# Kernel optimization log

Measured on AMD Instinct MI355X. Metric: run time of the kernel, lower is better.

Reference implementation:

```python
import jax, jax.numpy as jnp
import numpy as np

HIDDEN = 4096
N_HEADS = 32
HEAD_DIM = HIDDEN // N_HEADS  # 128
ROPE_BASE = 10000.0


def _rotate_half(x):
    h = x.shape[-1] // 2
    return jnp.concatenate((-x[..., h:], x[..., :h]), axis=-1)


def _rope_sin_cos(position_ids):
    # position_ids: [B, S] int -> sin, cos: [B, 1, S, head_dim]
    inv_freq = 1.0 / (ROPE_BASE ** (jnp.arange(0, HEAD_DIM, 2, dtype=jnp.float32) / HEAD_DIM))
    freqs = position_ids.astype(jnp.float32)[..., None] * inv_freq  # [B,S,hd/2]
    emb = jnp.concatenate((freqs, freqs), axis=-1)  # [B,S,hd]
    return jnp.sin(emb)[:, None, :, :], jnp.cos(emb)[:, None, :, :]


def setup_inputs() -> dict:
    key = jax.random.key(0)
    k1, k2, k3 = jax.random.split(key, 3)
    B, S = 2, 2048
    hidden_states = jax.random.normal(k1, (B, S, HIDDEN), dtype=jnp.float32)
    w_qkv = jax.random.normal(k2, (HIDDEN, 3 * HIDDEN), dtype=jnp.float32) * 0.02
    wo = jax.random.normal(k3, (HIDDEN, HIDDEN), dtype=jnp.float32) * 0.02
    position_ids = jnp.broadcast_to(jnp.arange(S, dtype=jnp.int32)[None, :], (B, S))
    return {"hidden_states": hidden_states, "w_qkv": w_qkv, "wo": wo,
            "position_ids": position_ids}


def reference(hidden_states, w_qkv, wo, position_ids):
    B, S, H = hidden_states.shape
    qkv = hidden_states @ w_qkv  # [B,S,3H]
    q, k, v = jnp.split(qkv, 3, axis=-1)
    # [B,S,nH,hd] -> [B,nH,S,hd]
    q = q.reshape(B, S, N_HEADS, HEAD_DIM).transpose(0, 2, 1, 3)
    k = k.reshape(B, S, N_HEADS, HEAD_DIM).transpose(0, 2, 1, 3)
    v = v.reshape(B, S, N_HEADS, HEAD_DIM).transpose(0, 2, 1, 3)
    sin, cos = _rope_sin_cos(position_ids)  # [B,1,S,hd]
    q = q * cos + _rotate_half(q) * sin
    k = k * cos + _rotate_half(k) * sin
    scale = 1.0 / np.sqrt(HEAD_DIM)
    scores = jnp.einsum('bhqd,bhkd->bhqk', q, k) * scale
    causal = jnp.tril(jnp.ones((S, S), dtype=bool))
    scores = jnp.where(causal[None, None, :, :], scores, jnp.finfo(scores.dtype).min)
    attn = jax.nn.softmax(scores, axis=-1)
    out = jnp.einsum('bhqk,bhkd->bhqd', attn, v)  # [B,nH,S,hd]
    out = out.transpose(0, 2, 1, 3).reshape(B, S, H)
    return out @ wo
```

## Files before the change

kernel.cpp:

```cpp
#include <hip/hip_runtime.h>

typedef unsigned int u32;
typedef unsigned short u16;
typedef short short8 __attribute__((ext_vector_type(8)));
typedef float f32x4 __attribute__((ext_vector_type(4)));
typedef unsigned short us4 __attribute__((ext_vector_type(4)));

#define S_LEN 2048
#define BATCH 2
#define HID 4096
#define NH 32
#define HD 128
#define TRIH 12288

#define GCAST(p) ((const __attribute__((address_space(1))) u32*)(p))
#define LCAST(p) ((__attribute__((address_space(3))) u32*)(p))

static __device__ __forceinline__ u16 f2bf(float f) {
  union { float f; u32 u; } x; x.f = f;
  u32 u = x.u;
  u32 r = u + 0x7FFFu + ((u >> 16) & 1u);
  return (u16)(r >> 16);
}
static __device__ __forceinline__ float bf2f(u16 h) {
  union { u32 u; float f; } x; x.u = ((u32)h) << 16;
  return x.f;
}

__global__ __launch_bounds__(256) void cvt_f32_bf16(const float* __restrict__ in,
                                                    u16* __restrict__ out, int n4) {
  int i = blockIdx.x * 256 + threadIdx.x;
  if (i >= n4) return;
  float4 v = ((const float4*)in)[i];
  us4 o;
  o.x = f2bf(v.x); o.y = f2bf(v.y); o.z = f2bf(v.z); o.w = f2bf(v.w);
  ((us4*)out)[i] = o;
}

__global__ __launch_bounds__(256) void tr_cvt(const float* __restrict__ in,
                                              u16* __restrict__ out, int R, int C) {
  __shared__ float tile[32][33];
  int c0 = blockIdx.x * 32, r0 = blockIdx.y * 32;
  int tx = threadIdx.x, ty = threadIdx.y;
  for (int i = ty; i < 32; i += 8)
    tile[i][tx] = in[(size_t)(r0 + i) * C + c0 + tx];
  __syncthreads();
  for (int i = ty; i < 32; i += 8)
    out[(size_t)(c0 + i) * R + r0 + tx] = f2bf(tile[tx][i]);
}


template<int MQ, int NQ>
static __device__ __forceinline__ void mfma_quad(f32x4 (&acc)[8][4], short8 (&af)[4][2],
                                                 short8 (&bfr)[4][2]) {
#pragma unroll
  for (int ml = 0; ml < 4; ++ml)
#pragma unroll
    for (int nl = 0; nl < 2; ++nl) {
      acc[MQ*4+ml][NQ*2+nl] = __builtin_amdgcn_mfma_f32_16x16x32_bf16(
          af[ml][0], bfr[NQ*2+nl][0], acc[MQ*4+ml][NQ*2+nl], 0, 0, 0);
      acc[MQ*4+ml][NQ*2+nl] = __builtin_amdgcn_mfma_f32_16x16x32_bf16(
          af[ml][1], bfr[NQ*2+nl][1], acc[MQ*4+ml][NQ*2+nl], 0, 0, 0);
    }
}

template<int MQ>
static __device__ __forceinline__ void read_a(short8 (&af)[4][2], const u16* abase, int lane) {
#pragma unroll
  for (int ml = 0; ml < 4; ++ml) {
    int r = MQ*64 + ml*16 + (lane & 15);
#pragma unroll
    for (int kh = 0; kh < 2; ++kh) {
      int j = kh*4 + (lane >> 4);
      af[ml][kh] = *(const short8*)(abase + r*64 + ((j ^ (r & 7)) << 3));
    }
  }
}
template<int NQ>
static __device__ __forceinline__ void read_b(short8 (&bfr)[4][2], const u16* bbase,
                                              int rbase, int lane) {
#pragma unroll
  for (int nl = 0; nl < 2; ++nl) {
    int r = rbase + (NQ*2+nl)*16 + (lane & 15);
#pragma unroll
    for (int kh = 0; kh < 2; ++kh) {
      int j = kh*4 + (lane >> 4);
      bfr[NQ*2+nl][kh] = *(const short8*)(bbase + r*64 + ((j ^ (r & 7)) << 3));
    }
  }
}

#define BAR_MFMA(MQX, NQX) \
  __builtin_amdgcn_s_barrier(); \
  asm volatile("s_waitcnt lgkmcnt(0)" ::: "memory"); \
  __builtin_amdgcn_sched_barrier(0); \
  __builtin_amdgcn_s_setprio(1); \
  mfma_quad<MQX, NQX>(acc, af, bfr); \
  __builtin_amdgcn_s_setprio(0); \
  __builtin_amdgcn_s_barrier();

#define BAR_MFMA_DRAIN(MQX, NQX, NSTR) \
  __builtin_amdgcn_s_barrier(); \
  asm volatile("s_waitcnt lgkmcnt(0)" ::: "memory"); \
  __builtin_amdgcn_sched_barrier(0); \
  __builtin_amdgcn_s_setprio(1); \
  mfma_quad<MQX, NQX>(acc, af, bfr); \
  __builtin_amdgcn_s_setprio(0); \
  asm volatile("s_waitcnt vmcnt(" NSTR ")" ::: "memory"); \
  __builtin_amdgcn_s_barrier(); \
  __builtin_amdgcn_sched_barrier(0);

template<int OUTF32>
__global__ __launch_bounds__(512, 1) void gemm256(const u16* __restrict__ A,
                                                  const u16* __restrict__ Bt,
                                                  void* __restrict__ Cout,
                                                  int M, int N, int K, int nbm) {
  __shared__ __attribute__((aligned(16))) u16 lds[65536];
  const int tid = threadIdx.x, wave = tid >> 6, lane = tid & 63;
  const int wr = wave >> 2, wc = wave & 3;
  const int nwg = gridDim.x, wg = blockIdx.x, cpx = nwg >> 3;
  const int swz = (wg & 7) * cpx + (wg >> 3);
  const size_t tileM = (size_t)(swz % nbm) * 256;
  const size_t tileN = (size_t)(swz / nbm) * 256;
  const int nIter = K >> 7;

  const int r_ = tid >> 3;
  const int gc_ = (tid & 7) ^ (r_ & 7);

  const u16* Ag = A + tileM * K;
  const u16* Bg = Bt + tileN * K;

  f32x4 acc[8][4] = {};
  short8 af[4][2], bfr[4][2];

  auto stageA = [&](int kt, int buf, int half) {
    const u16* g0 = Ag + (size_t)(half*128 + r_) * K + kt*64 + (gc_ << 3);
    u16* l = lds + buf*16384 + half*8192 + wave*512;
    __builtin_amdgcn_global_load_lds(GCAST(g0), LCAST(l), 16, 0, 0);
    __builtin_amdgcn_global_load_lds(GCAST(g0 + (size_t)64*K), LCAST(l + 4096), 16, 0, 0);
  };
  auto stageB = [&](int kt, int buf, int half) {
    const u16* g0 = Bg + (size_t)(half*128 + r_) * K + kt*64 + (gc_ << 3);
    u16* l = lds + 32768 + buf*16384 + half*8192 + wave*512;
    __builtin_amdgcn_global_load_lds(GCAST(g0), LCAST(l), 16, 0, 0);
    __builtin_amdgcn_global_load_lds(GCAST(g0 + (size_t)64*K), LCAST(l + 4096), 16, 0, 0);
  };

  const u16* a0 = lds + wr*8192;
  const u16* a1 = lds + 16384 + wr*8192;
  const u16* b0 = lds + 32768 + (wc >> 1)*8192;
  const u16* b1 = lds + 32768 + 16384 + (wc >> 1)*8192;
  const int brb = (wc & 1) * 64;

  stageA(0, 0, 0); stageA(0, 0, 1);
  stageB(0, 0, 0); stageB(0, 0, 1);
  stageB(1, 1, 0); stageB(1, 1, 1);
  asm volatile("s_waitcnt vmcnt(4)" ::: "memory");
  __builtin_amdgcn_s_barrier();
  __builtin_amdgcn_sched_barrier(0);

  for (int i = 0; i < nIter; ++i) {
    const int t1 = 2*i + 1, t2 = 2*i + 2, t3 = 2*i + 3;
    const bool more = (i + 1 < nIter);
    read_a<0>(af, a0, lane);
    read_b<0>(bfr, b0, brb, lane);
    stageA(t1, 1, 0);
    asm volatile("s_waitcnt lgkmcnt(8)" ::: "memory");
    BAR_MFMA(0, 0)
    read_b<1>(bfr, b0, brb, lane);
    stageA(t1, 1, 1);
    BAR_MFMA(0, 1)
    read_a<1>(af, a0, lane);
    if (more) stageB(t2, 0, 0);
    BAR_MFMA(1, 0)
    if (more) {
      stageB(t2, 0, 1);
      BAR_MFMA_DRAIN(1, 1, "4")
    } else {
      BAR_MFMA_DRAIN(1, 1, "0")
    }
    read_a<0>(af, a1, lane);
    read_b<0>(bfr, b1, brb, lane);
    if (more) stageA(t2, 0, 0);
    asm volatile("s_waitcnt lgkmcnt(8)" ::: "memory");
    BAR_MFMA(0, 0)
    read_b<1>(bfr, b1, brb, lane);
    if (more) stageA(t2, 0, 1);
    BAR_MFMA(0, 1)
    read_a<1>(af, a1, lane);
    if (more) stageB(t3, 1, 0);
    BAR_MFMA(1, 0)
    if (more) {
      stageB(t3, 1, 1);
      BAR_MFMA_DRAIN(1, 1, "4")
    } else {
      BAR_MFMA(1, 1)
    }
  }

  const int r0o = (lane >> 4) << 2, c0o = lane & 15;
#pragma unroll
  for (int m = 0; m < 8; ++m)
#pragma unroll
    for (int n = 0; n < 4; ++n)
#pragma unroll
      for (int rr = 0; rr < 4; ++rr) {
        size_t grow = tileM + wr*128 + m*16 + r0o + rr;
        size_t gcol = tileN + wc*64 + n*16 + c0o;
        if (OUTF32) ((float*)Cout)[grow * N + gcol] = acc[m][n][rr];
        else        ((u16*)Cout)[grow * N + gcol] = f2bf(acc[m][n][rr]);
      }
}

__global__ __launch_bounds__(256) void rope_kernel(u16* __restrict__ qkv,
                                                   const int* __restrict__ pid) {
  int idx = blockIdx.x * 256 + threadIdx.x;
  int row = idx >> 12;
  int rem = idx & 4095;
  int which = rem >> 11;
  int rem2 = rem & 2047;
  int h = rem2 >> 6;
  int j = rem2 & 63;
  u16* p = qkv + (size_t)row * TRIH + which * HID + h * HD + j;
  float x0 = bf2f(p[0]), x1 = bf2f(p[64]);
  float pos = (float)pid[row];
  float invf = expf(-(float)j * 0.14391156831212787f);
  float th = pos * invf;
  float sn, cs;
  sincosf(th, &sn, &cs);
  p[0]  = f2bf(x0 * cs - x1 * sn);
  p[64] = f2bf(x1 * cs + x0 * sn);
}

__global__ __launch_bounds__(512, 2) void attn_kernel(const u16* __restrict__ qkv,
                                                      u16* __restrict__ O) {
  const int bid = blockIdx.x;
  const int qt = 15 - (bid >> 6);
  const int bh = bid & 63;
  const int b = bh >> 5, h = bh & 31;
  const int tid = threadIdx.x, wave = tid >> 6, lane = tid & 63;
  __shared__ u16 Ks[64 * 128];
  __shared__ u16 VsT[128 * 64];
  __shared__ u16 Ps[8][16 * 64];
  const u16* base = qkv + (size_t)b * S_LEN * TRIH + h * HD;

  const int rbase = (lane >> 4) << 2;
  const int cbase = lane & 15;
  const int q_lo = qt * 128;
  const int wrow0 = q_lo + wave * 16;

  short8 qf[4];
  {
    const u16* qrow = base + (size_t)(wrow0 + cbase) * TRIH;
#pragma unroll
    for (int f = 0; f < 4; ++f)
      qf[f] = *(const short8*)(qrow + ((f * 4 + (lane >> 4)) << 3));
  }

  const int tmax_w = 2 * qt + (wave >= 4 ? 1 : 0);
  const int tmax_b = 2 * qt + 1;

  float mrun[4], lrun[4];
  f32x4 accO[8] = {};
#pragma unroll
  for (int r = 0; r < 4; ++r) { mrun[r] = -1e30f; lrun[r] = 0.f; }

  short8 kreg[2], vreg[2];
#pragma unroll
  for (int it = 0; it < 2; ++it) {
    int c = tid + it * 512;
    int row = c >> 4, ch = c & 15;
    const u16* src = base + (size_t)row * TRIH + (ch << 3);
    kreg[it] = *(const short8*)(src + HID);
    vreg[it] = *(const short8*)(src + 2 * HID);
  }

  for (int t = 0; t <= tmax_b; ++t) {
    __syncthreads();
#pragma unroll
    for (int it = 0; it < 2; ++it) {
      int c = tid + it * 512;
      int row = c >> 4, ch = c & 15;
      *(short8*)(Ks + row * 128 + ((ch ^ (row & 7)) << 3)) = kreg[it];
#pragma unroll
      for (int i = 0; i < 8; ++i) {
        int d = (ch << 3) + i;
        VsT[d * 64 + (((row >> 3) ^ (ch & 7)) << 3) + (row & 7)] = (u16)vreg[it][i];
      }
    }
    __syncthreads();

    if (t < tmax_b) {
      int kv1 = (t + 1) << 6;
#pragma unroll
      for (int it = 0; it < 2; ++it) {
        int c = tid + it * 512;
        int row = c >> 4, ch = c & 15;
        const u16* src = base + (size_t)(kv1 + row) * TRIH + (ch << 3);
        kreg[it] = *(const short8*)(src + HID);
        vreg[it] = *(const short8*)(src + 2 * HID);
      }
    }

    if (t > tmax_w) continue;

    f32x4 s[4] = {};
#pragma unroll
    for (int n = 0; n < 4; ++n) {
      int krow = n * 16 + cbase;
#pragma unroll
      for (int f = 0; f < 4; ++f) {
        int ch = f * 4 + (lane >> 4);
        short8 kf = *(const short8*)(Ks + krow * 128 + ((ch ^ (krow & 7)) << 3));
        s[n] = __builtin_amdgcn_mfma_f32_16x16x32_bf16(qf[f], kf, s[n], 0, 0, 0);
      }
    }
    const float scale = 0.08838834764831845f;
    const int kv0 = t << 6;
    if (t == tmax_w) {
#pragma unroll
      for (int n = 0; n < 4; ++n)
#pragma unroll
        for (int r = 0; r < 4; ++r) {
          int kvcol = kv0 + n * 16 + cbase;
          int qrow = wrow0 + rbase + r;
          s[n][r] = (kvcol <= qrow) ? s[n][r] * scale : -1e30f;
        }
    } else {
#pragma unroll
      for (int n = 0; n < 4; ++n) s[n] *= scale;
    }

    float tmax[4];
#pragma unroll
    for (int r = 0; r < 4; ++r) {
      float tm = fmaxf(fmaxf(s[0][r], s[1][r]), fmaxf(s[2][r], s[3][r]));
      tm = fmaxf(tm, __shfl_xor(tm, 1));
      tm = fmaxf(tm, __shfl_xor(tm, 2));
      tm = fmaxf(tm, __shfl_xor(tm, 4));
      tm = fmaxf(tm, __shfl_xor(tm, 8));
      tmax[r] = tm;
    }
    bool need = false;
#pragma unroll
    for (int r = 0; r < 4; ++r) need |= (tmax[r] > mrun[r] + 8.0f);
    if (__any(need)) {
#pragma unroll
      for (int r = 0; r < 4; ++r) {
        float mnew = fmaxf(mrun[r], tmax[r]);
        float corr = __expf(mrun[r] - mnew);
        float rs = 0.f;
#pragma unroll
        for (int n = 0; n < 4; ++n) { float pv = __expf(s[n][r] - mnew); s[n][r] = pv; rs += pv; }
        rs += __shfl_xor(rs, 1); rs += __shfl_xor(rs, 2);
        rs += __shfl_xor(rs, 4); rs += __shfl_xor(rs, 8);
        lrun[r] = lrun[r] * corr + rs;
        mrun[r] = mnew;
#pragma unroll
        for (int nd = 0; nd < 8; ++nd) accO[nd][r] *= corr;
      }
    } else {
#pragma unroll
      for (int r = 0; r < 4; ++r) {
        float rs = 0.f;
#pragma unroll
        for (int n = 0; n < 4; ++n) { float pv = __expf(s[n][r] - mrun[r]); s[n][r] = pv; rs += pv; }
        rs += __shfl_xor(rs, 1); rs += __shfl_xor(rs, 2);
        rs += __shfl_xor(rs, 4); rs += __shfl_xor(rs, 8);
        lrun[r] += rs;
      }
    }

    u16* Pw = (u16*)Ps[wave];
#pragma unroll
    for (int n = 0; n < 4; ++n)
#pragma unroll
      for (int r = 0; r < 4; ++r) {
        int rl = rbase + r;
        int col = n * 16 + cbase;
        Pw[rl * 64 + (((col >> 3) ^ (rl & 7)) << 3) + (col & 7)] = f2bf(s[n][r]);
      }

    short8 pa[2];
    {
      int prow = lane & 15;
#pragma unroll
      for (int f2 = 0; f2 < 2; ++f2) {
        int ch = f2 * 4 + (lane >> 4);
        pa[f2] = *(const short8*)(Pw + prow * 64 + ((ch ^ (prow & 7)) << 3));
      }
    }
#pragma unroll
    for (int nd = 0; nd < 8; ++nd) {
      int drow = nd * 16 + cbase;
#pragma unroll
      for (int f2 = 0; f2 < 2; ++f2) {
        int ch = f2 * 4 + (lane >> 4);
        short8 vb = *(const short8*)(VsT + drow * 64 + ((ch ^ ((drow >> 3) & 7)) << 3));
        accO[nd] = __builtin_amdgcn_mfma_f32_16x16x32_bf16(pa[f2], vb, accO[nd], 0, 0, 0);
      }
    }
  }

#pragma unroll
  for (int nd = 0; nd < 8; ++nd)
#pragma unroll
    for (int r = 0; r < 4; ++r) {
      int qrow = wrow0 + rbase + r;
      int col = h * HD + nd * 16 + cbase;
      O[(size_t)(b * S_LEN + qrow) * HID + col] = f2bf(accO[nd][r] / lrun[r]);
    }
}

extern "C" void kernel_launch(void* const* d_in, const int* in_sizes, int n_in,
                              void* d_out, int out_size, void* d_ws, size_t ws_size,
                              hipStream_t stream) {
  const float* hidden = (const float*)d_in[0];
  const float* w_qkv  = (const float*)d_in[1];
  const float* wo     = (const float*)d_in[2];
  const int*   pid    = (const int*)d_in[3];

  const size_t MB = 1024ull * 1024ull;
  u16* hb    = (u16*)d_ws;
  u16* wqkvT = (u16*)((char*)d_ws + 32 * MB);
  u16* woT   = (u16*)((char*)d_ws + 128 * MB);
  u16* qkvb  = (u16*)((char*)d_ws + 160 * MB);
  u16* Obuf  = hb;

  cvt_f32_bf16<<<16384, 256, 0, stream>>>(hidden, hb, (BATCH * S_LEN * HID) / 4);
  dim3 tb(32, 8);
  tr_cvt<<<dim3(TRIH / 32, HID / 32), tb, 0, stream>>>(w_qkv, wqkvT, HID, TRIH);
  tr_cvt<<<dim3(HID / 32, HID / 32), tb, 0, stream>>>(wo, woT, HID, HID);

  gemm256<0><<<768, 512, 0, stream>>>(hb, wqkvT, qkvb, BATCH * S_LEN, TRIH, HID, 16);

  rope_kernel<<<(BATCH * S_LEN * 2 * NH * 64) / 256, 256, 0, stream>>>(qkvb, pid);

  attn_kernel<<<1024, 512, 0, stream>>>(qkvb, Obuf);

  gemm256<1><<<256, 512, 0, stream>>>(Obuf, woT, d_out, BATCH * S_LEN, HID, HID, 16);
}
```

Before: 842.6 us.

## Merge GEMM MFMA phases to halve barriers per main-loop iteration

The 256x256 bf16 GEMM main loop goes from eight barrier-fenced MFMA quads per iteration to four phases, each running two quads back to back. Each phase issues its LDS fragment reads and global-to-LDS staging together, then closes with a single barrier. The explicit lgkmcnt waits and scheduling fences before each MFMA group are removed, so the compiler now places the LDS waits itself. The aim is to cut barrier and wait overhead, at the cost of less fine-grained overlap between LDS reads and MFMAs, and more fragment registers live at once.

```diff
diff --git a/kernel.cpp b/kernel.cpp
--- a/kernel.cpp
+++ b/kernel.cpp
@@ -90,22 +90,11 @@
   }
 }
 
-#define BAR_MFMA(MQX, NQX) \
+#define PHASE_CLOSE() \
   __builtin_amdgcn_s_barrier(); \
-  asm volatile("s_waitcnt lgkmcnt(0)" ::: "memory"); \
-  __builtin_amdgcn_sched_barrier(0); \
-  __builtin_amdgcn_s_setprio(1); \
-  mfma_quad<MQX, NQX>(acc, af, bfr); \
-  __builtin_amdgcn_s_setprio(0); \
-  __builtin_amdgcn_s_barrier();
-
-#define BAR_MFMA_DRAIN(MQX, NQX, NSTR) \
-  __builtin_amdgcn_s_barrier(); \
-  asm volatile("s_waitcnt lgkmcnt(0)" ::: "memory"); \
-  __builtin_amdgcn_sched_barrier(0); \
-  __builtin_amdgcn_s_setprio(1); \
-  mfma_quad<MQX, NQX>(acc, af, bfr); \
-  __builtin_amdgcn_s_setprio(0); \
+  __builtin_amdgcn_sched_barrier(0);
+
+#define SEAM_CLOSE(NSTR) \
   asm volatile("s_waitcnt vmcnt(" NSTR ")" ::: "memory"); \
   __builtin_amdgcn_s_barrier(); \
   __builtin_amdgcn_sched_barrier(0);
@@ -155,47 +144,47 @@
   stageA(0, 0, 0); stageA(0, 0, 1);
   stageB(0, 0, 0); stageB(0, 0, 1);
   stageB(1, 1, 0); stageB(1, 1, 1);
-  asm volatile("s_waitcnt vmcnt(4)" ::: "memory");
-  __builtin_amdgcn_s_barrier();
-  __builtin_amdgcn_sched_barrier(0);
+  SEAM_CLOSE("4")
 
   for (int i = 0; i < nIter; ++i) {
     const int t1 = 2*i + 1, t2 = 2*i + 2, t3 = 2*i + 3;
     const bool more = (i + 1 < nIter);
+
     read_a<0>(af, a0, lane);
     read_b<0>(bfr, b0, brb, lane);
-    stageA(t1, 1, 0);
-    asm volatile("s_waitcnt lgkmcnt(8)" ::: "memory");
-    BAR_MFMA(0, 0)
     read_b<1>(bfr, b0, brb, lane);
-    stageA(t1, 1, 1);
-    BAR_MFMA(0, 1)
+    stageA(t1, 1, 0); stageA(t1, 1, 1);
+    __builtin_amdgcn_s_setprio(1);
+    mfma_quad<0, 0>(acc, af, bfr);
+    mfma_quad<0, 1>(acc, af, bfr);
+    __builtin_amdgcn_s_setprio(0);
+    PHASE_CLOSE()
+
     read_a<1>(af, a0, lane);
-    if (more) stageB(t2, 0, 0);
-    BAR_MFMA(1, 0)
-    if (more) {
-      stageB(t2, 0, 1);
-      BAR_MFMA_DRAIN(1, 1, "4")
-    } else {
-      BAR_MFMA_DRAIN(1, 1, "0")
-    }
+    if (more) { stageB(t2, 0, 0); stageB(t2, 0, 1); }
+    __builtin_amdgcn_s_setprio(1);
+    mfma_quad<1, 0>(acc, af, bfr);
+    mfma_quad<1, 1>(acc, af, bfr);
+    __builtin_amdgcn_s_setprio(0);
+    if (more) { SEAM_CLOSE("4") } else { SEAM_CLOSE("0") }
+
     read_a<0>(af, a1, lane);
     read_b<0>(bfr, b1, brb, lane);
-    if (more) stageA(t2, 0, 0);
-    asm volatile("s_waitcnt lgkmcnt(8)" ::: "memory");
-    BAR_MFMA(0, 0)
     read_b<1>(bfr, b1, brb, lane);
-    if (more) stageA(t2, 0, 1);
-    BAR_MFMA(0, 1)
+    if (more) { stageA(t2, 0, 0); stageA(t2, 0, 1); }
+    __builtin_amdgcn_s_setprio(1);
+    mfma_quad<0, 0>(acc, af, bfr);
+    mfma_quad<0, 1>(acc, af, bfr);
+    __builtin_amdgcn_s_setprio(0);
+    PHASE_CLOSE()
+
     read_a<1>(af, a1, lane);
-    if (more) stageB(t3, 1, 0);
-    BAR_MFMA(1, 0)
-    if (more) {
-      stageB(t3, 1, 1);
-      BAR_MFMA_DRAIN(1, 1, "4")
-    } else {
-      BAR_MFMA(1, 1)
-    }
+    if (more) { stageB(t3, 1, 0); stageB(t3, 1, 1); }
+    __builtin_amdgcn_s_setprio(1);
+    mfma_quad<1, 0>(acc, af, bfr);
+    mfma_quad<1, 1>(acc, af, bfr);
+    __builtin_amdgcn_s_setprio(0);
+    if (more) { SEAM_CLOSE("4") } else { PHASE_CLOSE() }
   }
 
   const int r0o = (lane >> 4) << 2, c0o = lane & 15;
```

Result: faster. 822.0 us (-2.4%).
